# Optimization experiments

Measured on AMD Instinct MI355X. Metric: run time of the kernel, lower is better.

The kernel has to match this reference:

```python
import jax, jax.numpy as jnp
import numpy as np

D = 768      # d_model == d_patch (16*16*3)
DFF = 3072
NH = 12
DH = D // NH  # 64
P = 16
IMG = 224
HP = IMG // P  # 14
NP = HP * HP   # 196
L = NP + 1     # 197 with CLS
NL = 12        # layers (weights SHARED across layers, per original code)
NC = 1000


def _pos_enc(length, d):
    # Faithful to PositionalEncoding: even dims sin with exponent i, odd dims cos with exponent i-1
    pos = jnp.arange(length, dtype=jnp.float32)[:, None]          # [L,1]
    dim = jnp.arange(d)
    i = jnp.where(dim % 2 == 0, dim, (dim // 2) * 2).astype(jnp.float32)
    ang = pos / jnp.power(10000.0, i / d)                          # [L,D]
    return jnp.where(dim % 2 == 0, jnp.sin(ang), jnp.cos(ang))


def _ln(x, g, b, eps=1e-5):
    m = x.mean(-1, keepdims=True)
    v = x.var(-1, keepdims=True)
    return (x - m) / jnp.sqrt(v + eps) * g + b


def setup_inputs() -> dict:
    key = jax.random.key(0)
    ks = jax.random.split(key, 12)
    s = 0.02
    n = lambda k, shp: jax.random.normal(k, shp, jnp.float32) * s
    return {
        "x": jax.random.normal(ks[0], (32, 3, IMG, IMG), jnp.float32),
        "w_proj": n(ks[1], (D, D)), "b_proj": jnp.zeros((D,), jnp.float32),
        "cls_emb": jnp.zeros((1, 1, D), jnp.float32),
        "ln1_g": jnp.ones((D,), jnp.float32), "ln1_b": jnp.zeros((D,), jnp.float32),
        "w_qkv": n(ks[2], (3 * D, D)), "b_qkv": jnp.zeros((3 * D,), jnp.float32),
        "w_o": n(ks[3], (D, D)), "b_o": jnp.zeros((D,), jnp.float32),
        "ln2_g": jnp.ones((D,), jnp.float32), "ln2_b": jnp.zeros((D,), jnp.float32),
        "w_fc1": n(ks[4], (DFF, D)), "b_fc1": jnp.zeros((DFF,), jnp.float32),
        "w_fc2": n(ks[5], (D, DFF)), "b_fc2": jnp.zeros((D,), jnp.float32),
        "lnf_g": jnp.ones((D,), jnp.float32), "lnf_b": jnp.zeros((D,), jnp.float32),
        "w_h": n(ks[6], (D, D)), "b_h": jnp.zeros((D,), jnp.float32),
        "w_c": n(ks[7], (NC, D)), "b_c": jnp.zeros((NC,), jnp.float32),
    }


def reference(x, w_proj, b_proj, cls_emb, ln1_g, ln1_b, w_qkv, b_qkv, w_o, b_o,
              ln2_g, ln2_b, w_fc1, b_fc1, w_fc2, b_fc2, lnf_g, lnf_b,
              w_h, b_h, w_c, b_c):
    b = x.shape[0]
    # convert_to_patch: unfold -> channel-major patch features [b, NP, 3*P*P]
    patches = x.reshape(b, 3, HP, P, HP, P).transpose(0, 2, 4, 1, 3, 5).reshape(b, NP, 3 * P * P)
    emb = patches @ w_proj.T + b_proj                              # [b,NP,D]
    cls = jnp.broadcast_to(cls_emb, (b, 1, D))
    h = jnp.concatenate([cls, emb], axis=1) + _pos_enc(L, D)[None]  # [b,L,D]

    inv_sqrt_dk = 1.0 / jnp.sqrt(jnp.float32(DH))
    for _ in range(NL):  # SAME weights every layer (faithful to nn.Sequential of one object)
        y = _ln(h, ln1_g, ln1_b)
        qkv = y @ w_qkv.T + b_qkv                                   # [b,L,3D]
        # faithful non-standard head split: view(b,l,3*DH,NH).transpose -> [b,NH,L,3*DH]
        qkv = qkv.reshape(b, L, 3 * DH, NH).transpose(0, 3, 1, 2)
        q, k, v = jnp.split(qkv, 3, axis=-1)                        # each [b,NH,L,DH]
        attn = jax.nn.softmax(jnp.einsum('bhld,bhmd->bhlm', q, k) * inv_sqrt_dk, axis=-1)
        o = jnp.einsum('bhlm,bhmd->bhld', attn, v)                  # [b,NH,L,DH]
        o = o.transpose(0, 2, 1, 3).reshape(b, L, D)
        h = h + (o @ w_o.T + b_o)
        y = _ln(h, ln2_g, ln2_b)
        f = jax.nn.gelu(y @ w_fc1.T + b_fc1, approximate=False) @ w_fc2.T + b_fc2
        h = h + f

    rep = _ln(h[:, 0], lnf_g, lnf_b)                                # [b,D]
    hid = jnp.tanh(rep @ w_h.T + b_h)                               # is_pretrain=True
    return hid @ w_c.T + b_c                                        # [b,NC]
```

## Files before the change

### kernel.cpp

```cpp
#include <hip/hip_runtime.h>
#include <hip/hip_bf16.h>


typedef __bf16 bf16;
typedef __bf16 bf16x8 __attribute__((ext_vector_type(8)));
typedef __bf16 bf16x4 __attribute__((ext_vector_type(4)));
typedef float  f32x4  __attribute__((ext_vector_type(4)));

typedef __attribute__((address_space(1))) const unsigned int gu32;
typedef __attribute__((address_space(3))) unsigned int lu32;

static __device__ __forceinline__ f32x4 mfma_bf16(bf16x8 a, bf16x8 b, f32x4 c) {
  return __builtin_amdgcn_mfma_f32_16x16x32_bf16(a, b, c, 0, 0, 0);
}
static __device__ __forceinline__ void gll16(const bf16* g, bf16* l) {
  __builtin_amdgcn_global_load_lds((gu32*)g, (lu32*)l, 16, 0, 0);
}


__global__ __launch_bounds__(256) void f2b_k(const float* __restrict__ a, bf16* __restrict__ o, int n) {
  int i = blockIdx.x * 256 + threadIdx.x;
  if (i < n) o[i] = (bf16)a[i];
}

__global__ __launch_bounds__(256) void posenc_k(float* __restrict__ pos) {
  int l = blockIdx.x;
  for (int d = threadIdx.x; d < 768; d += 256) {
    int ieff = d & ~1;
    float ang = (float)l * expf(-(float)ieff * (9.210340371976184f / 768.0f));
    pos[l * 768 + d] = (d & 1) ? cosf(ang) : sinf(ang);
  }
}

__global__ __launch_bounds__(256) void patchify_k(const float* __restrict__ x, bf16* __restrict__ p) {
  int idx = blockIdx.x * 256 + threadIdx.x;
  int t = idx / 768, col = idx - t * 768;
  int b = t / 196, pp = t - b * 196;
  int ph = pp / 14, pw = pp - ph * 14;
  int c = col >> 8, r = col & 255, i = r >> 4, j = r & 15;
  p[idx] = (bf16)x[((b * 3 + c) * 224 + ph * 16 + i) * 224 + pw * 16 + j];
}

__global__ __launch_bounds__(256) void cls_k(float* __restrict__ h, const float* __restrict__ pos,
                                             const float* __restrict__ cls) {
  int b = blockIdx.x;
  for (int d = threadIdx.x; d < 768; d += 256)
    h[((size_t)b * 197) * 768 + d] = cls[d] + pos[d];
}

template<int PAD>
__global__ __launch_bounds__(256) void ln4_k(const float* __restrict__ x, const float* __restrict__ g,
                                             const float* __restrict__ bb, bf16* __restrict__ y,
                                             int nrows, int instride) {
  const int wave = threadIdx.x >> 6, lane = threadIdx.x & 63;
  const int row = blockIdx.x * 4 + wave;
  if (row >= nrows) return;
  const float4* x4 = (const float4*)(x + (size_t)row * instride);
  float4 v0 = x4[lane], v1 = x4[lane + 64], v2 = x4[lane + 128];
  float s  = v0.x + v0.y + v0.z + v0.w + v1.x + v1.y + v1.z + v1.w + v2.x + v2.y + v2.z + v2.w;
  float s2 = v0.x*v0.x + v0.y*v0.y + v0.z*v0.z + v0.w*v0.w
           + v1.x*v1.x + v1.y*v1.y + v1.z*v1.z + v1.w*v1.w
           + v2.x*v2.x + v2.y*v2.y + v2.z*v2.z + v2.w*v2.w;
  #pragma unroll
  for (int o = 1; o < 64; o <<= 1) { s += __shfl_xor(s, o); s2 += __shfl_xor(s2, o); }
  float m = s * (1.0f / 768.0f);
  float inv = rsqrtf(s2 * (1.0f / 768.0f) - m * m + 1e-5f);
  int orow = row;
  if (PAD) { int bq = row / 197; orow = row + bq * 3; }
  bf16* yr = y + (size_t)orow * 768;
  const float4* g4 = (const float4*)g;
  const float4* b4 = (const float4*)bb;
  #pragma unroll
  for (int i = 0; i < 3; ++i) {
    int idx = lane + i * 64;
    float4 vv = (i == 0) ? v0 : (i == 1) ? v1 : v2;
    float4 gv = g4[idx], bv = b4[idx];
    bf16x4 o;
    o[0] = (bf16)((vv.x - m) * inv * gv.x + bv.x);
    o[1] = (bf16)((vv.y - m) * inv * gv.y + bv.y);
    o[2] = (bf16)((vv.z - m) * inv * gv.z + bv.z);
    o[3] = (bf16)((vv.w - m) * inv * gv.w + bv.w);
    *(bf16x4*)(yr + idx * 4) = o;
  }
}

template<int BN, int EPI, bool DBUF>
__global__ __launch_bounds__(256, 2) void gemm2(
    const bf16* __restrict__ A, const bf16* __restrict__ B,
    int M, int N, int K, int ldc, int gx, int xfast, const float* __restrict__ bias,
    const float* __restrict__ posw,
    float* __restrict__ outF, bf16* __restrict__ outB)
{
  constexpr int WN = (BN == 256) ? 128 : 32;
  constexpr int NI = WN / 16;
  constexpr int NC = (NI > 4) ? 4 : NI;
  constexpr int NB = BN / 32;
  constexpr int NBUF = DBUF ? 2 : 1;
  __shared__ alignas(16) bf16 As[NBUF][128 * 64];
  __shared__ alignas(16) bf16 Bs[NBUF][BN * 64];
  const int tid = threadIdx.x;
  const int lane = tid & 63, wave = tid >> 6;
  const int wr = wave >> 1, wc = wave & 1;
  const int lrow = lane & 15, lgrp = lane >> 4;

  const int nwg = gridDim.x, bid0 = blockIdx.x;
  const int xcd = bid0 & 7, loc = bid0 >> 3;
  const int q = nwg >> 3, r = nwg & 7;
  const int nb = (xcd < r ? xcd * (q + 1) : r * (q + 1) + (xcd - r) * q) + loc;
  int bx, by;
  if (xfast) { bx = nb % gx; by = nb / gx; }
  else       { int gy = nwg / gx; by = nb % gy; bx = nb / gy; }
  const int row0 = bx * 128, col0 = by * BN;

  f32x4 acc[4][NI] = {};
  const int srow = lane >> 3, schunk = lane & 7;
  const int nk = K >> 6;

  const bf16* aptr[4];
  const bf16* bptr[NB];
  {
    const bf16* Agb = A + (size_t)row0 * K;
    const bf16* Bgb = B + (size_t)col0 * K;
    #pragma unroll
    for (int i = 0; i < 4; ++i) {
      int rr = (wave * 4 + i) * 8 + srow;
      aptr[i] = Agb + (size_t)rr * K + ((schunk ^ (rr & 7)) << 3);
    }
    #pragma unroll
    for (int i = 0; i < NB; ++i) {
      int rr = (wave * NB + i) * 8 + srow;
      bptr[i] = Bgb + (size_t)rr * K + ((schunk ^ (rr & 7)) << 3);
    }
  }
  int aoff[2][4], boff[2][NI];
  #pragma unroll
  for (int kk = 0; kk < 2; ++kk) {
    #pragma unroll
    for (int mi = 0; mi < 4; ++mi) {
      int rr = wr * 64 + mi * 16 + lrow;
      aoff[kk][mi] = rr * 64 + (((kk * 4 + lgrp) ^ (rr & 7)) << 3);
    }
    #pragma unroll
    for (int ni = 0; ni < NI; ++ni) {
      int rr = wc * WN + ni * 16 + lrow;
      boff[kk][ni] = rr * 64 + (((kk * 4 + lgrp) ^ (rr & 7)) << 3);
    }
  }

  auto stage = [&](int buf) {
    #pragma unroll
    for (int i = 0; i < 4; ++i) {
      gll16(aptr[i], As[buf] + (wave * 4 + i) * 512);
      aptr[i] += 64;
    }
    #pragma unroll
    for (int i = 0; i < NB; ++i) {
      gll16(bptr[i], Bs[buf] + (wave * NB + i) * 512);
      bptr[i] += 64;
    }
  };
  auto compute = [&](const bf16* Ac, const bf16* Bc) {
    #pragma unroll
    for (int kk = 0; kk < 2; ++kk) {
      bf16x8 af[4];
      #pragma unroll
      for (int mi = 0; mi < 4; ++mi) af[mi] = *(const bf16x8*)(Ac + aoff[kk][mi]);
      #pragma unroll
      for (int nh = 0; nh < NI / NC; ++nh) {
        bf16x8 bfr[NC];
        #pragma unroll
        for (int nj = 0; nj < NC; ++nj)
          bfr[nj] = *(const bf16x8*)(Bc + boff[kk][nh * NC + nj]);
        __builtin_amdgcn_s_setprio(1);
        #pragma unroll
        for (int mi = 0; mi < 4; ++mi)
          #pragma unroll
          for (int nj = 0; nj < NC; ++nj)
            acc[mi][nh * NC + nj] = mfma_bf16(af[mi], bfr[nj], acc[mi][nh * NC + nj]);
        __builtin_amdgcn_s_setprio(0);
      }
    }
  };

  if constexpr (DBUF) {
    stage(0);
    __syncthreads();
    int cur = 0;
    for (int kt = 0; kt < nk; ++kt) {
      if (kt + 1 < nk) stage(cur ^ 1);
      compute(As[cur], Bs[cur]);
      __syncthreads();
      cur ^= 1;
    }
  } else {
    for (int kt = 0; kt < nk; ++kt) {
      stage(0);
      __syncthreads();
      compute(As[0], Bs[0]);
      __syncthreads();
    }
  }

  #pragma unroll
  for (int ni = 0; ni < NI; ++ni) {
    const int col = col0 + wc * WN + ni * 16 + lrow;
    float bs = 0.0f;
    if (EPI != 1) {
      if (EPI == 5) bs = (col < N) ? bias[col] : 0.0f;
      else          bs = bias[col];
    }
    #pragma unroll
    for (int mi = 0; mi < 4; ++mi) {
      const int rbase = row0 + wr * 64 + mi * 16 + (lgrp << 2);
      #pragma unroll
      for (int j = 0; j < 4; ++j) {
        const int t = rbase + j;
        if (EPI == 1) {
          float val = acc[mi][ni][j] + bias[t];
          if (t < 768) val *= 0.125f;
          outB[(size_t)t * ldc + col] = (bf16)val;
        } else {
          if (t >= M) continue;
          float val = acc[mi][ni][j] + bs;
          if (EPI == 0) {
            int b = t / 196, p = t - b * 196;
            outF[((size_t)(b * 197 + 1 + p)) * 768 + col] = val + posw[(size_t)(1 + p) * 768 + col];
          } else if (EPI == 2) {
            outF[(size_t)t * 768 + col] += val;
          } else if (EPI == 3) {
            outB[(size_t)t * 3072 + col] = (bf16)(0.5f * val * (1.0f + erff(val * 0.70710678118654752f)));
          } else if (EPI == 4) {
            outB[(size_t)t * 768 + col] = (bf16)tanhf(val);
          } else {
            if (col < N) outF[(size_t)t * ldc + col] = val;
          }
        }
      }
    }
  }
}

__global__ __launch_bounds__(512) void attn_k(const bf16* __restrict__ Ct, bf16* __restrict__ O) {
  __shared__ alignas(16) bf16 Ks[208 * 64];
  __shared__ alignas(16) bf16 Qs[208 * 64];
  __shared__ alignas(16) bf16 Vs[64 * 232];
  __shared__ alignas(16) bf16 Ps[8][16 * 232];
  const int bh = blockIdx.x;
  const int b = bh / 12, hh = bh - b * 12;
  const int tid = threadIdx.x, lane = tid & 63, wave = tid >> 6;
  const int lrow = lane & 15, lgrp = lane >> 4;
  const size_t tc0 = (size_t)b * 200;

  for (int task = tid; task < 1600; task += 512) {
    int d = task / 25, lc = task - d * 25;
    int l0 = lc * 8;
    const size_t cb = tc0 + l0;
    bf16x8 qv = *(const bf16x8*)(Ct + ((size_t)(d * 12 + hh)) * 6400 + cb);
    bf16x8 kv = *(const bf16x8*)(Ct + ((size_t)(768 + d * 12 + hh)) * 6400 + cb);
    bf16x8 vv = *(const bf16x8*)(Ct + ((size_t)(1536 + d * 12 + hh)) * 6400 + cb);
    #pragma unroll
    for (int e = 0; e < 8; ++e) {
      int l = l0 + e;
      int sw = ((((d >> 3) ^ (l & 7)) << 3) | (d & 7));
      Ks[l * 64 + sw] = kv[e];
      Qs[l * 64 + sw] = qv[e];
    }
    *(bf16x8*)(Vs + d * 232 + l0) = vv;
  }
  for (int q = tid; q < 64 * 35; q += 512) {
    int d = q / 35, c = 197 + (q - d * 35);
    Vs[d * 232 + c] = (bf16)0.0f;
  }
  __syncthreads();

  for (int rt = wave; rt < 13; rt += 8) {
    const int r = rt * 16 + lrow;
    bf16x8 a0 = *(const bf16x8*)(Qs + r * 64 + ((lgrp ^ (r & 7)) << 3));
    bf16x8 a1 = *(const bf16x8*)(Qs + r * 64 + (((4 + lgrp) ^ (r & 7)) << 3));
    f32x4 sacc[13];
    #pragma unroll
    for (int ct = 0; ct < 13; ++ct) {
      const int kr = ct * 16 + lrow;
      bf16x8 b0 = *(const bf16x8*)(Ks + kr * 64 + ((lgrp ^ (kr & 7)) << 3));
      bf16x8 b1 = *(const bf16x8*)(Ks + kr * 64 + (((4 + lgrp) ^ (kr & 7)) << 3));
      f32x4 s = {};
      s = mfma_bf16(a0, b0, s);
      s = mfma_bf16(a1, b1, s);
      sacc[ct] = s;
    }
    bf16* Pw = Ps[wave];
    float inv4[4];
    #pragma unroll
    for (int j = 0; j < 4; ++j) {
      const int prow = (lgrp << 2) + j;
      float mx = -3.0e38f;
      #pragma unroll
      for (int ct = 0; ct < 13; ++ct) {
        int c = ct * 16 + lrow;
        if (c < 197) mx = fmaxf(mx, sacc[ct][j]);
      }
      #pragma unroll
      for (int o = 1; o < 16; o <<= 1) mx = fmaxf(mx, __shfl_xor(mx, o));
      float sum = 0.0f;
      #pragma unroll
      for (int ct = 0; ct < 13; ++ct) {
        int c = ct * 16 + lrow;
        float p = (c < 197) ? __expf(sacc[ct][j] - mx) : 0.0f;
        sum += p;
        Pw[prow * 232 + c] = (bf16)p;
      }
      #pragma unroll
      for (int o = 1; o < 16; o <<= 1) sum += __shfl_xor(sum, o);
      inv4[j] = 1.0f / sum;
      Pw[prow * 232 + 208 + lrow] = (bf16)0.0f;
    }
    f32x4 oacc[4] = {};
    #pragma unroll
    for (int mc = 0; mc < 7; ++mc) {
      bf16x8 pa = *(const bf16x8*)(Pw + lrow * 232 + mc * 32 + (lgrp << 3));
      #pragma unroll
      for (int n2 = 0; n2 < 4; ++n2) {
        bf16x8 vb = *(const bf16x8*)(Vs + (n2 * 16 + lrow) * 232 + mc * 32 + (lgrp << 3));
        oacc[n2] = mfma_bf16(pa, vb, oacc[n2]);
      }
    }
    #pragma unroll
    for (int n2 = 0; n2 < 4; ++n2) {
      const int d = n2 * 16 + lrow;
      #pragma unroll
      for (int j = 0; j < 4; ++j) {
        const int qrow = rt * 16 + (lgrp << 2) + j;
        if (qrow < 197)
          O[((size_t)b * 197 + qrow) * 768 + hh * 64 + d] = (bf16)(oacc[n2][j] * inv4[j]);
      }
    }
  }
}


extern "C" void kernel_launch(void* const* d_in, const int* in_sizes, int n_in,
                              void* d_out, int out_size, void* d_ws, size_t ws_size,
                              hipStream_t stream) {
  const float* x      = (const float*)d_in[0];
  const float* w_proj = (const float*)d_in[1];
  const float* b_proj = (const float*)d_in[2];
  const float* cls    = (const float*)d_in[3];
  const float* ln1g   = (const float*)d_in[4];
  const float* ln1b   = (const float*)d_in[5];
  const float* w_qkv  = (const float*)d_in[6];
  const float* b_qkv  = (const float*)d_in[7];
  const float* w_o    = (const float*)d_in[8];
  const float* b_o    = (const float*)d_in[9];
  const float* ln2g   = (const float*)d_in[10];
  const float* ln2b   = (const float*)d_in[11];
  const float* w_fc1  = (const float*)d_in[12];
  const float* b_fc1  = (const float*)d_in[13];
  const float* w_fc2  = (const float*)d_in[14];
  const float* b_fc2  = (const float*)d_in[15];
  const float* lnfg   = (const float*)d_in[16];
  const float* lnfb   = (const float*)d_in[17];
  const float* w_h    = (const float*)d_in[18];
  const float* b_h    = (const float*)d_in[19];
  const float* w_c    = (const float*)d_in[20];
  const float* b_c    = (const float*)d_in[21];
  float* out = (float*)d_out;

  uint8_t* ws = (uint8_t*)d_ws;
  size_t off = 0;
  auto alloc = [&](size_t bytes) -> void* {
    void* p = ws + off; off += (bytes + 255) & ~(size_t)255; return p;
  };
  float* h    = (float*)alloc(6400ull * 768 * 4);
  bf16*  ybf  = (bf16*) alloc(6400ull * 768 * 2);
  bf16*  ct   = (bf16*) alloc(2304ull * 6400 * 2);
  bf16*  ob   = (bf16*) alloc(6400ull * 768 * 2);
  bf16*  f1   = (bf16*) alloc(6400ull * 3072 * 2);
  float* pos  = (float*)alloc(197ull * 768 * 4);
  bf16* wprojB = (bf16*)alloc(768ull * 768 * 2);
  bf16* wqkvB  = (bf16*)alloc(2304ull * 768 * 2);
  bf16* woB    = (bf16*)alloc(768ull * 768 * 2);
  bf16* wfc1B  = (bf16*)alloc(3072ull * 768 * 2);
  bf16* wfc2B  = (bf16*)alloc(768ull * 3072 * 2);
  bf16* whB    = (bf16*)alloc(768ull * 768 * 2);
  bf16* wcB    = (bf16*)alloc(1024ull * 768 * 2);
  bf16* repB   = (bf16*)alloc(128ull * 768 * 2);
  bf16* hidB   = (bf16*)alloc(128ull * 768 * 2);
  bf16* patches = f1;

  f2b_k<<<(768 * 768 + 255) / 256, 256, 0, stream>>>(w_proj, wprojB, 768 * 768);
  f2b_k<<<(2304 * 768 + 255) / 256, 256, 0, stream>>>(w_qkv, wqkvB, 2304 * 768);
  f2b_k<<<(768 * 768 + 255) / 256, 256, 0, stream>>>(w_o, woB, 768 * 768);
  f2b_k<<<(3072 * 768 + 255) / 256, 256, 0, stream>>>(w_fc1, wfc1B, 3072 * 768);
  f2b_k<<<(768 * 3072 + 255) / 256, 256, 0, stream>>>(w_fc2, wfc2B, 768 * 3072);
  f2b_k<<<(768 * 768 + 255) / 256, 256, 0, stream>>>(w_h, whB, 768 * 768);
  f2b_k<<<(1000 * 768 + 255) / 256, 256, 0, stream>>>(w_c, wcB, 1000 * 768);
  posenc_k<<<197, 256, 0, stream>>>(pos);
  patchify_k<<<6272 * 768 / 256, 256, 0, stream>>>(x, patches);
  gemm2<64, 0, true><<<49 * 12, 256, 0, stream>>>(patches, wprojB, 6272, 768, 768, 768, 49, 0,
                                                  b_proj, pos, h, nullptr);
  cls_k<<<32, 256, 0, stream>>>(h, pos, cls);

  for (int layer = 0; layer < 12; ++layer) {
    ln4_k<1><<<1576, 256, 0, stream>>>(h, ln1g, ln1b, ybf, 6304, 768);
    gemm2<256, 1, false><<<18 * 25, 256, 0, stream>>>(wqkvB, ybf, 2304, 6400, 768, 6400, 18, 1,
                                                      b_qkv, nullptr, nullptr, ct);
    attn_k<<<384, 512, 0, stream>>>(ct, ob);
    gemm2<64, 2, true><<<50 * 12, 256, 0, stream>>>(ob, woB, 6304, 768, 768, 768, 50, 0,
                                                    b_o, nullptr, h, nullptr);
    ln4_k<0><<<1576, 256, 0, stream>>>(h, ln2g, ln2b, ybf, 6304, 768);
    gemm2<256, 3, false><<<50 * 12, 256, 0, stream>>>(ybf, wfc1B, 6304, 3072, 768, 3072, 50, 0,
                                                      b_fc1, nullptr, nullptr, f1);
    gemm2<64, 2, true><<<50 * 12, 256, 0, stream>>>(f1, wfc2B, 6304, 768, 3072, 768, 50, 0,
                                                    b_fc2, nullptr, h, nullptr);
  }

  ln4_k<0><<<8, 256, 0, stream>>>(h, lnfg, lnfb, repB, 32, 197 * 768);
  gemm2<64, 4, true><<<1 * 12, 256, 0, stream>>>(repB, whB, 32, 768, 768, 768, 1, 0,
                                                 b_h, nullptr, nullptr, hidB);
  gemm2<64, 5, true><<<1 * 16, 256, 0, stream>>>(hidB, wcB, 32, 1000, 768, 1000, 1, 0,
                                                 b_c, nullptr, out, nullptr);
}
```

Measured before the change: 2.935 ms.

## Double-buffer all GEMMs with vmcnt-based waits and shrink wide tiles to 128

All GEMM variants now use a double-buffered LDS pipeline. The next tile's async global-to-LDS loads are issued before computing the current one, with explicit s_waitcnt vmcnt counts and raw s_barrier replacing __syncthreads. The 256-wide tiles for the QKV and FC1 GEMMs become 128-wide, which doubles the grid and keeps the LDS footprint reasonable with two buffers. This aims to hide global load latency and raise occupancy. The cost is more blocks re-reading shared operands, and the hand-tuned vmcnt counts must match the number of loads issued per stage.

```diff
diff --git a/kernel.cpp b/kernel.cpp
--- a/kernel.cpp
+++ b/kernel.cpp
@@ -84,20 +84,18 @@
   }
 }
 
-template<int BN, int EPI, bool DBUF>
+template<int BN, int EPI>
 __global__ __launch_bounds__(256, 2) void gemm2(
     const bf16* __restrict__ A, const bf16* __restrict__ B,
     int M, int N, int K, int ldc, int gx, int xfast, const float* __restrict__ bias,
     const float* __restrict__ posw,
     float* __restrict__ outF, bf16* __restrict__ outB)
 {
-  constexpr int WN = (BN == 256) ? 128 : 32;
+  constexpr int WN = (BN == 128) ? 64 : 32;
   constexpr int NI = WN / 16;
-  constexpr int NC = (NI > 4) ? 4 : NI;
   constexpr int NB = BN / 32;
-  constexpr int NBUF = DBUF ? 2 : 1;
-  __shared__ alignas(16) bf16 As[NBUF][128 * 64];
-  __shared__ alignas(16) bf16 Bs[NBUF][BN * 64];
+  __shared__ alignas(16) bf16 As[2][128 * 64];
+  __shared__ alignas(16) bf16 Bs[2][BN * 64];
   const int tid = threadIdx.x;
   const int lane = tid & 63, wave = tid >> 6;
   const int wr = wave >> 1, wc = wave & 1;
@@ -162,43 +160,36 @@
   auto compute = [&](const bf16* Ac, const bf16* Bc) {
     #pragma unroll
     for (int kk = 0; kk < 2; ++kk) {
-      bf16x8 af[4];
+      bf16x8 af[4], bfr[NI];
       #pragma unroll
       for (int mi = 0; mi < 4; ++mi) af[mi] = *(const bf16x8*)(Ac + aoff[kk][mi]);
       #pragma unroll
-      for (int nh = 0; nh < NI / NC; ++nh) {
-        bf16x8 bfr[NC];
+      for (int ni = 0; ni < NI; ++ni) bfr[ni] = *(const bf16x8*)(Bc + boff[kk][ni]);
+      __builtin_amdgcn_s_setprio(1);
+      #pragma unroll
+      for (int mi = 0; mi < 4; ++mi)
         #pragma unroll
-        for (int nj = 0; nj < NC; ++nj)
-          bfr[nj] = *(const bf16x8*)(Bc + boff[kk][nh * NC + nj]);
-        __builtin_amdgcn_s_setprio(1);
-        #pragma unroll
-        for (int mi = 0; mi < 4; ++mi)
-          #pragma unroll
-          for (int nj = 0; nj < NC; ++nj)
-            acc[mi][nh * NC + nj] = mfma_bf16(af[mi], bfr[nj], acc[mi][nh * NC + nj]);
-        __builtin_amdgcn_s_setprio(0);
-      }
+        for (int ni = 0; ni < NI; ++ni)
+          acc[mi][ni] = mfma_bf16(af[mi], bfr[ni], acc[mi][ni]);
+      __builtin_amdgcn_s_setprio(0);
     }
   };
 
-  if constexpr (DBUF) {
-    stage(0);
-    __syncthreads();
-    int cur = 0;
-    for (int kt = 0; kt < nk; ++kt) {
-      if (kt + 1 < nk) stage(cur ^ 1);
-      compute(As[cur], Bs[cur]);
-      __syncthreads();
-      cur ^= 1;
-    }
-  } else {
-    for (int kt = 0; kt < nk; ++kt) {
-      stage(0);
-      __syncthreads();
-      compute(As[0], Bs[0]);
-      __syncthreads();
-    }
+  stage(0);
+  int cur = 0;
+  for (int kt = 0; kt < nk; ++kt) {
+    if (kt + 1 < nk) {
+      stage(cur ^ 1);
+      if constexpr (BN == 128) asm volatile("s_waitcnt vmcnt(8)" ::: "memory");
+      else                     asm volatile("s_waitcnt vmcnt(6)" ::: "memory");
+    } else {
+      asm volatile("s_waitcnt vmcnt(0)" ::: "memory");
+    }
+    __builtin_amdgcn_sched_barrier(0);
+    __builtin_amdgcn_s_barrier();
+    compute(As[cur], Bs[cur]);
+    __builtin_amdgcn_s_barrier();
+    cur ^= 1;
   }
 
   #pragma unroll
@@ -396,27 +387,27 @@
   f2b_k<<<(1000 * 768 + 255) / 256, 256, 0, stream>>>(w_c, wcB, 1000 * 768);
   posenc_k<<<197, 256, 0, stream>>>(pos);
   patchify_k<<<6272 * 768 / 256, 256, 0, stream>>>(x, patches);
-  gemm2<64, 0, true><<<49 * 12, 256, 0, stream>>>(patches, wprojB, 6272, 768, 768, 768, 49, 0,
-                                                  b_proj, pos, h, nullptr);
+  gemm2<64, 0><<<49 * 12, 256, 0, stream>>>(patches, wprojB, 6272, 768, 768, 768, 49, 0,
+                                            b_proj, pos, h, nullptr);
   cls_k<<<32, 256, 0, stream>>>(h, pos, cls);
 
   for (int layer = 0; layer < 12; ++layer) {
     ln4_k<1><<<1576, 256, 0, stream>>>(h, ln1g, ln1b, ybf, 6304, 768);
-    gemm2<256, 1, false><<<18 * 25, 256, 0, stream>>>(wqkvB, ybf, 2304, 6400, 768, 6400, 18, 1,
-                                                      b_qkv, nullptr, nullptr, ct);
+    gemm2<128, 1><<<18 * 50, 256, 0, stream>>>(wqkvB, ybf, 2304, 6400, 768, 6400, 18, 1,
+                                               b_qkv, nullptr, nullptr, ct);
     attn_k<<<384, 512, 0, stream>>>(ct, ob);
-    gemm2<64, 2, true><<<50 * 12, 256, 0, stream>>>(ob, woB, 6304, 768, 768, 768, 50, 0,
-                                                    b_o, nullptr, h, nullptr);
+    gemm2<64, 2><<<50 * 12, 256, 0, stream>>>(ob, woB, 6304, 768, 768, 768, 50, 0,
+                                              b_o, nullptr, h, nullptr);
     ln4_k<0><<<1576, 256, 0, stream>>>(h, ln2g, ln2b, ybf, 6304, 768);
-    gemm2<256, 3, false><<<50 * 12, 256, 0, stream>>>(ybf, wfc1B, 6304, 3072, 768, 3072, 50, 0,
-                                                      b_fc1, nullptr, nullptr, f1);
-    gemm2<64, 2, true><<<50 * 12, 256, 0, stream>>>(f1, wfc2B, 6304, 768, 3072, 768, 50, 0,
-                                                    b_fc2, nullptr, h, nullptr);
+    gemm2<128, 3><<<50 * 24, 256, 0, stream>>>(ybf, wfc1B, 6304, 3072, 768, 3072, 50, 0,
+                                               b_fc1, nullptr, nullptr, f1);
+    gemm2<64, 2><<<50 * 12, 256, 0, stream>>>(f1, wfc2B, 6304, 768, 3072, 768, 50, 0,
+                                              b_fc2, nullptr, h, nullptr);
   }
 
   ln4_k<0><<<8, 256, 0, stream>>>(h, lnfg, lnfb, repB, 32, 197 * 768);
-  gemm2<64, 4, true><<<1 * 12, 256, 0, stream>>>(repB, whB, 32, 768, 768, 768, 1, 0,
-                                                 b_h, nullptr, nullptr, hidB);
-  gemm2<64, 5, true><<<1 * 16, 256, 0, stream>>>(hidB, wcB, 32, 1000, 768, 1000, 1, 0,
-                                                 b_c, nullptr, out, nullptr);
-}
+  gemm2<64, 4><<<1 * 12, 256, 0, stream>>>(repB, whB, 32, 768, 768, 768, 1, 0,
+                                           b_h, nullptr, nullptr, hidB);
+  gemm2<64, 5><<<1 * 16, 256, 0, stream>>>(hidB, wcB, 32, 1000, 768, 1000, 1, 0,
+                                           b_c, nullptr, out, nullptr);
+}
```

Result: no change. 2.922 ms (-0.4%).
